# Optimization experiments

Measured on AMD Instinct MI355X. Metric: run time of the kernel, lower is better.

Reference implementation:

```python
import jax, jax.numpy as jnp
import numpy as np
from jax import lax
from jax.scipy.special import logsumexp

B, T, H, L = 64, 512, 768, 9


def setup_inputs() -> dict:
    key = jax.random.key(0)
    k1, k2, k3, k4, k5 = jax.random.split(key, 5)
    hidden = jax.random.normal(k1, (B, T, H), dtype=jnp.float32)
    W = jax.random.normal(k2, (L, H), dtype=jnp.float32) * 0.02
    b = jnp.zeros((L,), dtype=jnp.float32)
    transitions = jax.random.normal(k3, (L, L), dtype=jnp.float32) * 0.1
    lengths = jax.random.randint(k4, (B,), T // 2, T + 1)
    seq_mask = jnp.arange(T)[None, :] < lengths[:, None]          # [B,T] bool
    labels = jax.random.randint(k5, (B, T), 0, L).astype(jnp.int32)
    labels = jnp.where(seq_mask, labels, -100).astype(jnp.int32)   # -100 = ignore
    attention_mask = seq_mask.astype(jnp.int32)
    return {"hidden": hidden, "W": W, "b": b, "transitions": transitions,
            "labels": labels, "attention_mask": attention_mask}


def _crf_nll(logits, tags, transitions, mask):
    # numerator: joint score of the gold path (no start/end transitions)
    maskf = mask.astype(logits.dtype)
    emit = jnp.take_along_axis(logits, tags[..., None], axis=2)[..., 0]   # [B,T]
    emit_score = (emit * maskf).sum(-1)
    trans = transitions[tags[:, :-1], tags[:, 1:]]                        # [B,T-1]
    trans_score = (trans * maskf[:, 1:]).sum(-1)
    numerator = emit_score + trans_score
    # denominator: forward algorithm (log-sum-exp recurrence over time)
    def step(alpha, xs):
        logit_t, mask_t = xs                                   # [B,L], [B]
        inner = alpha[:, :, None] + transitions[None, :, :] + logit_t[:, None, :]
        new = logsumexp(inner, axis=1)
        return jnp.where(mask_t[:, None], new, alpha), None
    alpha0 = logits[:, 0]                                      # mask[:,0] assumed True
    alpha, _ = lax.scan(step, alpha0,
                        (jnp.transpose(logits[:, 1:], (1, 0, 2)), mask[:, 1:].T))
    denominator = logsumexp(alpha, axis=-1)
    return -(numerator - denominator).sum()


def _viterbi(logits, transitions, mask):
    num_tags = transitions.shape[0]
    identity_bp = jnp.broadcast_to(jnp.arange(num_tags)[None, :], logits.shape[:1] + (num_tags,))

    def vstep(vscore, xs):
        logit_t, mask_t = xs
        inner = vscore[:, :, None] + transitions[None, :, :]   # [B,L_prev,L_cur]
        bp = jnp.argmax(inner, axis=1)                         # [B,L]
        new = jnp.max(inner, axis=1) + logit_t
        vscore = jnp.where(mask_t[:, None], new, vscore)
        bp = jnp.where(mask_t[:, None], bp, identity_bp)       # carry tag through pad
        return vscore, bp

    vscore0 = logits[:, 0]
    vscore, bps = lax.scan(vstep, vscore0,
                           (jnp.transpose(logits[:, 1:], (1, 0, 2)), mask[:, 1:].T))
    last_tag = jnp.argmax(vscore, axis=-1)                     # [B]

    def btstep(tag, bp_t):
        prev = jnp.take_along_axis(bp_t, tag[:, None], axis=1)[:, 0]
        return prev, tag

    first_tag, tags_rest = lax.scan(btstep, last_tag, bps, reverse=True)  # ys[t]=tag_{t+1}
    return jnp.concatenate([first_tag[:, None], tags_rest.T], axis=1)     # [B,T]


def reference(hidden, W, b, transitions, labels, attention_mask):
    mask = (attention_mask != 0) & (labels != -100)            # create_combined_mask
    logits = jnp.einsum('bth,lh->btl', hidden, W) + b          # classifier (dropout=eval)
    tags = jnp.where(labels == -100, 0, labels)                # adjust_labels_for_crf
    loss = _crf_nll(logits, tags, transitions, mask)           # -log_likelihood (summed)
    vtags = _viterbi(logits, transitions, mask)                # [B,T]
    # pad_predictions: prepend -100, shift right, -100 outside the masked span
    bsz = hidden.shape[0]
    neg = jnp.full((bsz, 1), -100, dtype=jnp.int32)
    shifted = jnp.concatenate([neg, vtags[:, :-1].astype(jnp.int32)], axis=1)
    valid = jnp.concatenate([jnp.zeros((bsz, 1), bool), mask[:, :-1]], axis=1)
    predictions = jnp.where(valid, shifted, -100)
    return loss, predictions
```

## Files before the change

### kernel.cpp

```cpp
#include <hip/hip_runtime.h>

#define BATCH 64
#define TLEN  512
#define HDIM  768
#define LTAGS 9

#define WS_LOGD 0
#define WS_LOGF 2359296
#define WS_VM   3538944
#define WS_AM   6193152
#define WS_NUM  6856704
#define WS_LOSS 6857216

__global__ __launch_bounds__(256) void logits_kernel(
    const float* __restrict__ hidden, const float* __restrict__ W,
    const float* __restrict__ bvec, double* __restrict__ logitsD,
    float* __restrict__ logitsF)
{
    __shared__ float sW[LTAGS * HDIM];
    __shared__ float sb[LTAGS];
    const int tid = threadIdx.x;
    for (int i = tid; i < LTAGS * HDIM; i += 256) sW[i] = W[i];
    if (tid < LTAGS) sb[tid] = bvec[tid];
    __syncthreads();

    const int lane = tid & 63;
    const int wave = tid >> 6;
    const int sub  = lane & 7;
    const int rg   = lane >> 3;

    const int rowBase = blockIdx.x * 64 + wave * 16;
    const int r0 = rowBase + rg;
    const int r1 = rowBase + rg + 8;
    const float* h0p = hidden + (size_t)r0 * HDIM;
    const float* h1p = hidden + (size_t)r1 * HDIM;

    double acc0[LTAGS], acc1[LTAGS];
    #pragma unroll
    for (int l = 0; l < LTAGS; ++l) { acc0[l] = 0.0; acc1[l] = 0.0; }

    #pragma unroll 2
    for (int i = 0; i < 24; ++i) {
        const int off = i * 32 + sub * 4;
        const float4 h0 = *(const float4*)(h0p + off);
        const float4 h1 = *(const float4*)(h1p + off);
        #pragma unroll
        for (int l = 0; l < LTAGS; ++l) {
            const float4 w = *(const float4*)&sW[l * HDIM + off];
            float d0 = h0.x * w.x;
            d0 = fmaf(h0.y, w.y, d0); d0 = fmaf(h0.z, w.z, d0); d0 = fmaf(h0.w, w.w, d0);
            float d1 = h1.x * w.x;
            d1 = fmaf(h1.y, w.y, d1); d1 = fmaf(h1.z, w.z, d1); d1 = fmaf(h1.w, w.w, d1);
            acc0[l] += (double)d0;
            acc1[l] += (double)d1;
        }
    }
    #pragma unroll
    for (int l = 0; l < LTAGS; ++l) {
        double v0 = acc0[l], v1 = acc1[l];
        #pragma unroll
        for (int off = 4; off > 0; off >>= 1) {
            v0 += __shfl_down(v0, off);
            v1 += __shfl_down(v1, off);
        }
        acc0[l] = v0; acc1[l] = v1;
    }
    if (sub == 0) {
        #pragma unroll
        for (int l = 0; l < LTAGS; ++l) {
            double v0 = acc0[l] + (double)sb[l];
            double v1 = acc1[l] + (double)sb[l];
            logitsD[(size_t)r0 * LTAGS + l] = v0;
            logitsD[(size_t)r1 * LTAGS + l] = v1;
            logitsF[(size_t)r0 * LTAGS + l] = (float)v0;
            logitsF[(size_t)r1 * LTAGS + l] = (float)v1;
        }
    }
}

__global__ __launch_bounds__(256) void chunk_kernel(
    const float* __restrict__ trans, const int* __restrict__ labels,
    const int* __restrict__ att, const double* __restrict__ logitsD,
    const float* __restrict__ logitsF,
    double* __restrict__ wsVM, float* __restrict__ wsAM,
    double* __restrict__ wsNum)
{
    __shared__ double sT64[81];
    __shared__ float  sE32[81];
    const int tid = threadIdx.x;
    if (tid < 81) { float tv = trans[tid]; sT64[tid] = (double)tv; sE32[tid] = __expf(tv); }
    __syncthreads();

    const int blk = blockIdx.x;
    if (blk < 144) {
        const int gid = blk * 256 + tid;
        const int b   = gid / 576;
        const int rem = gid - b * 576;
        const int c   = rem / 9;
        const int i   = rem - c * 9;

        double M[LTAGS];
        #pragma unroll
        for (int j = 0; j < LTAGS; ++j) M[j] = (i == j) ? 0.0 : -1e300;

        const double* lrow = logitsD + ((size_t)b * TLEN + (c * 8 + 1)) * LTAGS;
        const int* lab = labels + b * TLEN;
        const int* am  = att + b * TLEN;
        const int t0 = c * 8 + 1;

        double lg[LTAGS], lgN[LTAGS];
        #pragma unroll
        for (int j = 0; j < LTAGS; ++j) lg[j] = lrow[j];
        bool mk = (am[t0] != 0) && (lab[t0] != -100);

        for (int s = 0; s < 8; ++s) {
            bool mkN = false;
            const int tn = t0 + s + 1;
            if (s < 7 && tn <= TLEN - 1) {
                const double* ln = lrow + (s + 1) * LTAGS;
                #pragma unroll
                for (int j = 0; j < LTAGS; ++j) lgN[j] = ln[j];
                mkN = (am[tn] != 0) && (lab[tn] != -100);
            }
            double nw[LTAGS];
            #pragma unroll
            for (int j = 0; j < LTAGS; ++j) {
                double bst = M[0] + sT64[j];
                #pragma unroll
                for (int k = 1; k < LTAGS; ++k) {
                    double cnd = M[k] + sT64[k * LTAGS + j];
                    bst = fmax(bst, cnd);
                }
                nw[j] = bst + lg[j];
            }
            #pragma unroll
            for (int j = 0; j < LTAGS; ++j) { M[j] = mk ? nw[j] : M[j]; lg[j] = lgN[j]; }
            mk = mkN;
        }
        double* dst = wsVM + (((size_t)b * 64 + c) * LTAGS + i) * LTAGS;
        #pragma unroll
        for (int j = 0; j < LTAGS; ++j) dst[j] = M[j];
    } else if (blk < 216) {
        const int gid = (blk - 144) * 256 + tid;
        const int b   = gid / 288;
        const int rem = gid - b * 288;
        const int c   = rem / 9;
        const int i   = rem - c * 9;

        float M[LTAGS];
        #pragma unroll
        for (int j = 0; j < LTAGS; ++j) M[j] = (i == j) ? 0.f : -1e30f;

        const float* lrow = logitsF + ((size_t)b * TLEN + (c * 16 + 1)) * LTAGS;
        const int* lab = labels + b * TLEN;
        const int* am  = att + b * TLEN;
        const int t0 = c * 16 + 1;

        float lg[LTAGS], lgN[LTAGS];
        #pragma unroll
        for (int j = 0; j < LTAGS; ++j) lg[j] = lrow[j];
        bool mk = (am[t0] != 0) && (lab[t0] != -100);

        for (int s = 0; s < 16; ++s) {
            bool mkN = false;
            const int tn = t0 + s + 1;
            if (s < 15 && tn <= TLEN - 1) {
                const float* ln = lrow + (s + 1) * LTAGS;
                #pragma unroll
                for (int j = 0; j < LTAGS; ++j) lgN[j] = ln[j];
                mkN = (am[tn] != 0) && (lab[tn] != -100);
            }
            float m = M[0];
            #pragma unroll
            for (int k = 1; k < LTAGS; ++k) m = fmaxf(m, M[k]);
            float P[LTAGS];
            #pragma unroll
            for (int k = 0; k < LTAGS; ++k) P[k] = __expf(M[k] - m);
            float nw[LTAGS];
            #pragma unroll
            for (int j = 0; j < LTAGS; ++j) {
                float sacc = P[0] * sE32[j];
                #pragma unroll
                for (int k = 1; k < LTAGS; ++k) sacc = fmaf(P[k], sE32[k * LTAGS + j], sacc);
                nw[j] = m + __logf(sacc) + lg[j];
            }
            #pragma unroll
            for (int j = 0; j < LTAGS; ++j) { M[j] = mk ? nw[j] : M[j]; lg[j] = lgN[j]; }
            mk = mkN;
        }
        float* dst = wsAM + (((size_t)b * 32 + c) * LTAGS + i) * LTAGS;
        #pragma unroll
        for (int j = 0; j < LTAGS; ++j) dst[j] = M[j];
    } else {
        const int bb   = (blk - 216) * 4 + (tid >> 6);
        const int lane = tid & 63;
        const int* lab = labels + bb * TLEN;
        const int* am  = att + bb * TLEN;
        const double* lrowb = logitsD + (size_t)bb * TLEN * LTAGS;
        double part = 0.0;
        #pragma unroll
        for (int k = 0; k < 8; ++k) {
            const int t = lane + k * 64;
            int lv = lab[t], av = am[t];
            bool mkc = (av != 0) && (lv != -100);
            int tg = (lv == -100) ? 0 : lv;
            if (mkc) part += lrowb[(size_t)t * LTAGS + tg];
            if (t < TLEN - 1) {
                int lv2 = lab[t + 1], av2 = am[t + 1];
                bool mk2 = (av2 != 0) && (lv2 != -100);
                int tg2 = (lv2 == -100) ? 0 : lv2;
                if (mk2) part += sT64[tg * LTAGS + tg2];
            }
        }
        #pragma unroll
        for (int off = 32; off > 0; off >>= 1) part += __shfl_down(part, off);
        if (lane == 0) wsNum[bb] = part;
    }
}

__global__ __launch_bounds__(128) void crf2_kernel(
    const float* __restrict__ trans, const int* __restrict__ labels,
    const int* __restrict__ att, const double* __restrict__ logitsD,
    const double* __restrict__ wsVM, const float* __restrict__ wsAM,
    const double* __restrict__ wsNum, double* __restrict__ wsLoss,
    float* __restrict__ out)
{
    __shared__ __align__(16) double sVM[64 * 81];
    __shared__ __align__(16) float  sAM[32 * 81];
    __shared__ double sVstart[65 * LTAGS];
    __shared__ unsigned long long sBPp[513];
    __shared__ int sTagB[65];
    __shared__ double sT64[81];
    __shared__ unsigned char sMk[513];
    __shared__ double sDen;
    __shared__ int sLast;

    const int b = blockIdx.x, tid = threadIdx.x;
    const int wave = tid >> 6, lane = tid & 63;
    const unsigned long long IDMAP = 0x876543210ull;

    const double2* gVM = (const double2*)(wsVM + (size_t)b * 64 * 81);
    double2* sVM2 = (double2*)sVM;
    for (int i = tid; i < 2592; i += 128) sVM2[i] = gVM[i];
    const float4* gAM = (const float4*)(wsAM + (size_t)b * 32 * 81);
    float4* sAM4 = (float4*)sAM;
    for (int i = tid; i < 648; i += 128) sAM4[i] = gAM[i];

    const int* lab = labels + b * TLEN;
    const int* am  = att + b * TLEN;
    for (int t = tid; t < TLEN; t += 128) {
        int lv = lab[t], av = am[t];
        sMk[t] = (av != 0 && lv != -100) ? 1 : 0;
    }
    if (tid == 0) sMk[TLEN] = 0;
    if (tid < 81) sT64[tid] = (double)trans[tid];
    __syncthreads();

    if (wave == 0) {
        const int j = (lane < LTAGS) ? lane : (LTAGS - 1);
        double v = logitsD[(size_t)b * TLEN * LTAGS + j];
        double Mc[LTAGS], Mn[LTAGS];
        #pragma unroll
        for (int i = 0; i < LTAGS; ++i) Mc[i] = sVM[i * LTAGS + j];
        for (int c = 0; c < 64; ++c) {
            if (c < 63) {
                #pragma unroll
                for (int i = 0; i < LTAGS; ++i) Mn[i] = sVM[(c + 1) * 81 + i * LTAGS + j];
            }
            if (lane < LTAGS) sVstart[c * LTAGS + j] = v;
            double g[LTAGS];
            #pragma unroll
            for (int i = 0; i < LTAGS; ++i) g[i] = __shfl(v, i);
            double bst = g[0] + Mc[0];
            #pragma unroll
            for (int i = 1; i < LTAGS; ++i) bst = fmax(bst, g[i] + Mc[i]);
            v = bst;
            if (c < 63) {
                #pragma unroll
                for (int i = 0; i < LTAGS; ++i) Mc[i] = Mn[i];
            }
        }
        if (lane < LTAGS) sVstart[64 * LTAGS + j] = v;
        double g[LTAGS];
        #pragma unroll
        for (int i = 0; i < LTAGS; ++i) g[i] = __shfl(v, i);
        if (lane == 0) {
            int bi = 0; double bv = g[0];
            #pragma unroll
            for (int i = 1; i < LTAGS; ++i) if (g[i] > bv) { bv = g[i]; bi = i; }
            sLast = bi;
        }
    } else {
        const int j = (lane < LTAGS) ? lane : (LTAGS - 1);
        float v = (float)logitsD[(size_t)b * TLEN * LTAGS + j];
        float Mc[LTAGS], Mn[LTAGS];
        #pragma unroll
        for (int i = 0; i < LTAGS; ++i) Mc[i] = sAM[i * LTAGS + j];
        for (int c = 0; c < 32; ++c) {
            if (c < 31) {
                #pragma unroll
                for (int i = 0; i < LTAGS; ++i) Mn[i] = sAM[(c + 1) * 81 + i * LTAGS + j];
            }
            float g[LTAGS];
            #pragma unroll
            for (int i = 0; i < LTAGS; ++i) g[i] = __shfl(v, i);
            float a[LTAGS];
            #pragma unroll
            for (int i = 0; i < LTAGS; ++i) a[i] = g[i] + Mc[i];
            float m = a[0];
            #pragma unroll
            for (int i = 1; i < LTAGS; ++i) m = fmaxf(m, a[i]);
            float sacc = 0.f;
            #pragma unroll
            for (int i = 0; i < LTAGS; ++i) sacc += __expf(a[i] - m);
            v = m + __logf(sacc);
            if (c < 31) {
                #pragma unroll
                for (int i = 0; i < LTAGS; ++i) Mc[i] = Mn[i];
            }
        }
        float g[LTAGS];
        #pragma unroll
        for (int i = 0; i < LTAGS; ++i) g[i] = __shfl(v, i);
        if (lane == 0) {
            float m = g[0];
            #pragma unroll
            for (int i = 1; i < LTAGS; ++i) m = fmaxf(m, g[i]);
            float sacc = 0.f;
            #pragma unroll
            for (int i = 0; i < LTAGS; ++i) sacc += __expf(g[i] - m);
            sDen = (double)(m + __logf(sacc));
        }
    }
    __syncthreads();

    unsigned long long S = IDMAP;
    if (tid < 64) {
        const int c = tid;
        double v[LTAGS];
        #pragma unroll
        for (int j = 0; j < LTAGS; ++j) v[j] = sVstart[c * LTAGS + j];
        const double* lrow = logitsD + ((size_t)b * TLEN + (c * 8 + 1)) * LTAGS;
        double lg[LTAGS], lgN[LTAGS];
        #pragma unroll
        for (int j = 0; j < LTAGS; ++j) lg[j] = lrow[j];

        for (int s = 0; s < 8; ++s) {
            const int t = c * 8 + 1 + s;
            if (s < 7 && t + 1 <= TLEN - 1) {
                const double* ln = lrow + (s + 1) * LTAGS;
                #pragma unroll
                for (int j = 0; j < LTAGS; ++j) lgN[j] = ln[j];
            }
            const bool mk = (sMk[t] != 0);
            unsigned long long pk = 0;
            double nv[LTAGS];
            #pragma unroll
            for (int j = 0; j < LTAGS; ++j) {
                double bst = v[0] + sT64[j];
                int bi = 0;
                #pragma unroll
                for (int k = 1; k < LTAGS; ++k) {
                    double cnd = v[k] + sT64[k * LTAGS + j];
                    bool gt = cnd > bst;
                    bst = gt ? cnd : bst;
                    bi  = gt ? k : bi;
                }
                nv[j] = bst + lg[j];
                pk |= ((unsigned long long)bi) << (4 * j);
            }
            pk = mk ? pk : IDMAP;
            sBPp[t] = pk;
            #pragma unroll
            for (int j = 0; j < LTAGS; ++j) { v[j] = mk ? nv[j] : v[j]; lg[j] = lgN[j]; }
        }
        unsigned long long G = IDMAP;
        for (int s = 7; s >= 0; --s) {
            const unsigned long long bp = sBPp[c * 8 + 1 + s];
            unsigned long long ng = 0;
            #pragma unroll
            for (int j = 0; j < LTAGS; ++j) {
                int gj = (int)((G >> (4 * j)) & 15);
                int f  = (int)((bp >> (4 * gj)) & 15);
                ng |= ((unsigned long long)f) << (4 * j);
            }
            G = ng;
        }
        S = G;
    }

    #pragma unroll
    for (int d = 1; d < 64; d <<= 1) {
        unsigned long long Sn = __shfl_down(S, d);
        if (wave == 0 && lane + d < 64) {
            unsigned long long R = 0;
            #pragma unroll
            for (int x = 0; x < LTAGS; ++x) {
                int y = (int)((Sn >> (4 * x)) & 15);
                int z = (int)((S >> (4 * y)) & 15);
                R |= ((unsigned long long)z) << (4 * x);
            }
            S = R;
        }
    }
    if (tid < 64) {
        const int lt = sLast;
        sTagB[tid] = (int)((S >> (4 * lt)) & 15);
        if (tid == 0) sTagB[64] = lt;
    }
    __syncthreads();

    if (tid < 64) {
        const int c = tid;
        int cur = sTagB[c + 1];
        float* po = out + 1 + b * TLEN;
        for (int s = 8; s >= 1; --s) {
            const int t = c * 8 + s;
            if (t < TLEN) {
                int nxt = (int)((sBPp[t] >> (4 * cur)) & 15);
                po[t] = sMk[t - 1] ? (float)nxt : -100.f;
                cur = nxt;
            }
        }
    }
    if (tid == 0) {
        out[1 + b * TLEN] = -100.f;
        wsLoss[b] = sDen - wsNum[b];
    }
}

__global__ __launch_bounds__(64) void loss_kernel(
    const double* __restrict__ wsLoss, float* __restrict__ out)
{
    double v = wsLoss[threadIdx.x];
    #pragma unroll
    for (int off = 32; off > 0; off >>= 1) v += __shfl_down(v, off);
    if (threadIdx.x == 0) out[0] = (float)v;
}

extern "C" void kernel_launch(void* const* d_in, const int* in_sizes, int n_in,
                              void* d_out, int out_size, void* d_ws, size_t ws_size,
                              hipStream_t stream)
{
    const float* hidden = (const float*)d_in[0];
    const float* W      = (const float*)d_in[1];
    const float* bvec   = (const float*)d_in[2];
    const float* trans  = (const float*)d_in[3];
    const int*   labels = (const int*)d_in[4];
    const int*   att    = (const int*)d_in[5];
    float* out = (float*)d_out;

    char* ws = (char*)d_ws;
    double* logitsD = (double*)(ws + WS_LOGD);
    float*  logitsF = (float*)(ws + WS_LOGF);
    double* wsVM    = (double*)(ws + WS_VM);
    float*  wsAM    = (float*)(ws + WS_AM);
    double* wsNum   = (double*)(ws + WS_NUM);
    double* wsLoss  = (double*)(ws + WS_LOSS);

    logits_kernel<<<512, 256, 0, stream>>>(hidden, W, bvec, logitsD, logitsF);
    chunk_kernel<<<232, 256, 0, stream>>>(trans, labels, att, logitsD, logitsF,
                                          wsVM, wsAM, wsNum);
    crf2_kernel<<<BATCH, 128, 0, stream>>>(trans, labels, att, logitsD,
                                           wsVM, wsAM, wsNum, wsLoss, out);
    loss_kernel<<<1, 64, 0, stream>>>(wsLoss, out);
}
```

Measured before the change: 217.9 us.

## Fuse chunk and CRF combine kernels into one per-batch block kernel

```diff
diff --git a/kernel.cpp b/kernel.cpp
--- a/kernel.cpp
+++ b/kernel.cpp
@@ -6,16 +6,11 @@
 #define LTAGS 9
 
 #define WS_LOGD 0
-#define WS_LOGF 2359296
-#define WS_VM   3538944
-#define WS_AM   6193152
-#define WS_NUM  6856704
-#define WS_LOSS 6857216
+#define WS_LOSS 2359296
 
 __global__ __launch_bounds__(256) void logits_kernel(
     const float* __restrict__ hidden, const float* __restrict__ W,
-    const float* __restrict__ bvec, double* __restrict__ logitsD,
-    float* __restrict__ logitsF)
+    const float* __restrict__ bvec, double* __restrict__ logitsD)
 {
     __shared__ float sW[LTAGS * HDIM];
     __shared__ float sb[LTAGS];
@@ -68,50 +63,81 @@
     if (sub == 0) {
         #pragma unroll
         for (int l = 0; l < LTAGS; ++l) {
-            double v0 = acc0[l] + (double)sb[l];
-            double v1 = acc1[l] + (double)sb[l];
-            logitsD[(size_t)r0 * LTAGS + l] = v0;
-            logitsD[(size_t)r1 * LTAGS + l] = v1;
-            logitsF[(size_t)r0 * LTAGS + l] = (float)v0;
-            logitsF[(size_t)r1 * LTAGS + l] = (float)v1;
+            logitsD[(size_t)r0 * LTAGS + l] = acc0[l] + (double)sb[l];
+            logitsD[(size_t)r1 * LTAGS + l] = acc1[l] + (double)sb[l];
         }
     }
 }
 
-__global__ __launch_bounds__(256) void chunk_kernel(
+__global__ __launch_bounds__(576) void crf_fused(
     const float* __restrict__ trans, const int* __restrict__ labels,
     const int* __restrict__ att, const double* __restrict__ logitsD,
-    const float* __restrict__ logitsF,
-    double* __restrict__ wsVM, float* __restrict__ wsAM,
-    double* __restrict__ wsNum)
+    double* __restrict__ wsLoss, float* __restrict__ out)
 {
+    __shared__ __align__(16) double sVM[64 * 81];
+    __shared__ __align__(16) float  sAM[32 * 81];
+    __shared__ double sVstart[65 * LTAGS];
+    __shared__ unsigned long long sBPp[513];
     __shared__ double sT64[81];
     __shared__ float  sE32[81];
-    const int tid = threadIdx.x;
+    __shared__ unsigned char sMk[513];
+    __shared__ int sTagB[65];
+    __shared__ double sRedN[9];
+    __shared__ double sNum, sDen;
+    __shared__ int sLast;
+
+    const int b = blockIdx.x, tid = threadIdx.x;
+    const int wave = tid >> 6, lane = tid & 63;
+    const unsigned long long IDMAP = 0x876543210ull;
+
+    const int* lab = labels + b * TLEN;
+    const int* am  = att + b * TLEN;
+    const double* gLD = logitsD + (size_t)b * TLEN * LTAGS;
+
     if (tid < 81) { float tv = trans[tid]; sT64[tid] = (double)tv; sE32[tid] = __expf(tv); }
+    if (tid < TLEN) {
+        int lv = lab[tid], av = am[tid];
+        sMk[tid] = (av != 0 && lv != -100) ? 1 : 0;
+    }
+    if (tid == 0) sMk[TLEN] = 0;
+
+    double part = 0.0;
+    if (tid < TLEN) {
+        const int t = tid;
+        int lv = lab[t], av = am[t];
+        bool mkc = (av != 0) && (lv != -100);
+        int tg = (lv == -100) ? 0 : lv;
+        if (mkc) part += gLD[(size_t)t * LTAGS + tg];
+        if (t < TLEN - 1) {
+            int lv2 = lab[t + 1], av2 = am[t + 1];
+            bool mk2 = (av2 != 0) && (lv2 != -100);
+            int tg2 = (lv2 == -100) ? 0 : lv2;
+            if (mk2) part += (double)trans[tg * LTAGS + tg2];
+        }
+    }
+    #pragma unroll
+    for (int off = 32; off > 0; off >>= 1) part += __shfl_down(part, off);
+    if (lane == 0) sRedN[wave] = part;
     __syncthreads();
-
-    const int blk = blockIdx.x;
-    if (blk < 144) {
-        const int gid = blk * 256 + tid;
-        const int b   = gid / 576;
-        const int rem = gid - b * 576;
-        const int c   = rem / 9;
-        const int i   = rem - c * 9;
-
+    if (tid == 0) {
+        double s = 0.0;
+        for (int w = 0; w < 9; ++w) s += sRedN[w];
+        sNum = s;
+    }
+
+    {
+        const int c = tid / 9, i = tid - 9 * c;
         double M[LTAGS];
         #pragma unroll
         for (int j = 0; j < LTAGS; ++j) M[j] = (i == j) ? 0.0 : -1e300;
 
-        const double* lrow = logitsD + ((size_t)b * TLEN + (c * 8 + 1)) * LTAGS;
-        const int* lab = labels + b * TLEN;
-        const int* am  = att + b * TLEN;
+        const double* lrow = gLD + (size_t)(c * 8 + 1) * LTAGS;
         const int t0 = c * 8 + 1;
 
         double lg[LTAGS], lgN[LTAGS];
         #pragma unroll
         for (int j = 0; j < LTAGS; ++j) lg[j] = lrow[j];
-        bool mk = (am[t0] != 0) && (lab[t0] != -100);
+        bool mk = (sMk[t0] != 0);
 
         for (int s = 0; s < 8; ++s) {
             bool mkN = false;
@@ -120,7 +146,7 @@
                 const double* ln = lrow + (s + 1) * LTAGS;
                 #pragma unroll
                 for (int j = 0; j < LTAGS; ++j) lgN[j] = ln[j];
-                mkN = (am[tn] != 0) && (lab[tn] != -100);
+                mkN = (sMk[tn] != 0);
             }
             double nw[LTAGS];
             #pragma unroll
@@ -137,38 +163,68 @@
             for (int j = 0; j < LTAGS; ++j) { M[j] = mk ? nw[j] : M[j]; lg[j] = lgN[j]; }
             mk = mkN;
         }
-        double* dst = wsVM + (((size_t)b * 64 + c) * LTAGS + i) * LTAGS;
-        #pragma unroll
-        for (int j = 0; j < LTAGS; ++j) dst[j] = M[j];
-    } else if (blk < 216) {
-        const int gid = (blk - 144) * 256 + tid;
-        const int b   = gid / 288;
-        const int rem = gid - b * 288;
-        const int c   = rem / 9;
-        const int i   = rem - c * 9;
-
+        #pragma unroll
+        for (int j = 0; j < LTAGS; ++j) sVM[c * 81 + i * LTAGS + j] = M[j];
+    }
+    __syncthreads();
+
+    if (wave == 0) {
+        const int j = (lane < LTAGS) ? lane : (LTAGS - 1);
+        double v = gLD[j];
+        double Mc[LTAGS], Mn[LTAGS];
+        #pragma unroll
+        for (int i = 0; i < LTAGS; ++i) Mc[i] = sVM[i * LTAGS + j];
+        for (int c = 0; c < 64; ++c) {
+            if (c < 63) {
+                #pragma unroll
+                for (int i = 0; i < LTAGS; ++i) Mn[i] = sVM[(c + 1) * 81 + i * LTAGS + j];
+            }
+            if (lane < LTAGS) sVstart[c * LTAGS + j] = v;
+            double g[LTAGS];
+            #pragma unroll
+            for (int i = 0; i < LTAGS; ++i) g[i] = __shfl(v, i);
+            double bst = g[0] + Mc[0];
+            #pragma unroll
+            for (int i = 1; i < LTAGS; ++i) bst = fmax(bst, g[i] + Mc[i]);
+            v = bst;
+            if (c < 63) {
+                #pragma unroll
+                for (int i = 0; i < LTAGS; ++i) Mc[i] = Mn[i];
+            }
+        }
+        if (lane < LTAGS) sVstart[64 * LTAGS + j] = v;
+        double g[LTAGS];
+        #pragma unroll
+        for (int i = 0; i < LTAGS; ++i) g[i] = __shfl(v, i);
+        if (lane == 0) {
+            int bi = 0; double bv = g[0];
+            #pragma unroll
+            for (int i = 1; i < LTAGS; ++i) if (g[i] > bv) { bv = g[i]; bi = i; }
+            sLast = bi;
+        }
+    } else if (tid >= 64 && tid < 352) {
+        const int idx = tid - 64;
+        const int c = idx / 9, i = idx - 9 * c;
         float M[LTAGS];
         #pragma unroll
         for (int j = 0; j < LTAGS; ++j) M[j] = (i == j) ? 0.f : -1e30f;
 
-        const float* lrow = logitsF + ((size_t)b * TLEN + (c * 16 + 1)) * LTAGS;
-        const int* lab = labels + b * TLEN;
-        const int* am  = att + b * TLEN;
+        const double* lrow = gLD + (size_t)(c * 16 + 1) * LTAGS;
         const int t0 = c * 16 + 1;
 
         float lg[LTAGS], lgN[LTAGS];
         #pragma unroll
-        for (int j = 0; j < LTAGS; ++j) lg[j] = lrow[j];
-        bool mk = (am[t0] != 0) && (lab[t0] != -100);
+        for (int j = 0; j < LTAGS; ++j) lg[j] = (float)lrow[j];
+        bool mk = (sMk[t0] != 0);
 
         for (int s = 0; s < 16; ++s) {
             bool mkN = false;
             const int tn = t0 + s + 1;
             if (s < 15 && tn <= TLEN - 1) {
-                const float* ln = lrow + (s + 1) * LTAGS;
-                #pragma unroll
-                for (int j = 0; j < LTAGS; ++j) lgN[j] = ln[j];
-                mkN = (am[tn] != 0) && (lab[tn] != -100);
+                const double* ln = lrow + (s + 1) * LTAGS;
+                #pragma unroll
+                for (int j = 0; j < LTAGS; ++j) lgN[j] = (float)ln[j];
+                mkN = (sMk[tn] != 0);
             }
             float m = M[0];
             #pragma unroll
@@ -188,159 +244,18 @@
             for (int j = 0; j < LTAGS; ++j) { M[j] = mk ? nw[j] : M[j]; lg[j] = lgN[j]; }
             mk = mkN;
         }
-        float* dst = wsAM + (((size_t)b * 32 + c) * LTAGS + i) * LTAGS;
-        #pragma unroll
-        for (int j = 0; j < LTAGS; ++j) dst[j] = M[j];
-    } else {
-        const int bb   = (blk - 216) * 4 + (tid >> 6);
-        const int lane = tid & 63;
-        const int* lab = labels + bb * TLEN;
-        const int* am  = att + bb * TLEN;
-        const double* lrowb = logitsD + (size_t)bb * TLEN * LTAGS;
-        double part = 0.0;
-        #pragma unroll
-        for (int k = 0; k < 8; ++k) {
-            const int t = lane + k * 64;
-            int lv = lab[t], av = am[t];
-            bool mkc = (av != 0) && (lv != -100);
-            int tg = (lv == -100) ? 0 : lv;
-            if (mkc) part += lrowb[(size_t)t * LTAGS + tg];
-            if (t < TLEN - 1) {
-                int lv2 = lab[t + 1], av2 = am[t + 1];
-                bool mk2 = (av2 != 0) && (lv2 != -100);
-                int tg2 = (lv2 == -100) ? 0 : lv2;
-                if (mk2) part += sT64[tg * LTAGS + tg2];
-            }
-        }
-        #pragma unroll
-        for (int off = 32; off > 0; off >>= 1) part += __shfl_down(part, off);
-        if (lane == 0) wsNum[bb] = part;
-    }
-}
-
-__global__ __launch_bounds__(128) void crf2_kernel(
-    const float* __restrict__ trans, const int* __restrict__ labels,
-    const int* __restrict__ att, const double* __restrict__ logitsD,
-    const double* __restrict__ wsVM, const float* __restrict__ wsAM,
-    const double* __restrict__ wsNum, double* __restrict__ wsLoss,
-    float* __restrict__ out)
-{
-    __shared__ __align__(16) double sVM[64 * 81];
-    __shared__ __align__(16) float  sAM[32 * 81];
-    __shared__ double sVstart[65 * LTAGS];
-    __shared__ unsigned long long sBPp[513];
-    __shared__ int sTagB[65];
-    __shared__ double sT64[81];
-    __shared__ unsigned char sMk[513];
-    __shared__ double sDen;
-    __shared__ int sLast;
-
-    const int b = blockIdx.x, tid = threadIdx.x;
-    const int wave = tid >> 6, lane = tid & 63;
-    const unsigned long long IDMAP = 0x876543210ull;
-
-    const double2* gVM = (const double2*)(wsVM + (size_t)b * 64 * 81);
-    double2* sVM2 = (double2*)sVM;
-    for (int i = tid; i < 2592; i += 128) sVM2[i] = gVM[i];
-    const float4* gAM = (const float4*)(wsAM + (size_t)b * 32 * 81);
-    float4* sAM4 = (float4*)sAM;
-    for (int i = tid; i < 648; i += 128) sAM4[i] = gAM[i];
-
-    const int* lab = labels + b * TLEN;
-    const int* am  = att + b * TLEN;
-    for (int t = tid; t < TLEN; t += 128) {
-        int lv = lab[t], av = am[t];
-        sMk[t] = (av != 0 && lv != -100) ? 1 : 0;
-    }
-    if (tid == 0) sMk[TLEN] = 0;
-    if (tid < 81) sT64[tid] = (double)trans[tid];
+        #pragma unroll
+        for (int j = 0; j < LTAGS; ++j) sAM[c * 81 + i * LTAGS + j] = M[j];
+    }
     __syncthreads();
 
+    unsigned long long S = IDMAP;
     if (wave == 0) {
-        const int j = (lane < LTAGS) ? lane : (LTAGS - 1);
-        double v = logitsD[(size_t)b * TLEN * LTAGS + j];
-        double Mc[LTAGS], Mn[LTAGS];
-        #pragma unroll
-        for (int i = 0; i < LTAGS; ++i) Mc[i] = sVM[i * LTAGS + j];
-        for (int c = 0; c < 64; ++c) {
-            if (c < 63) {
-                #pragma unroll
-                for (int i = 0; i < LTAGS; ++i) Mn[i] = sVM[(c + 1) * 81 + i * LTAGS + j];
-            }
-            if (lane < LTAGS) sVstart[c * LTAGS + j] = v;
-            double g[LTAGS];
-            #pragma unroll
-            for (int i = 0; i < LTAGS; ++i) g[i] = __shfl(v, i);
-            double bst = g[0] + Mc[0];
-            #pragma unroll
-            for (int i = 1; i < LTAGS; ++i) bst = fmax(bst, g[i] + Mc[i]);
-            v = bst;
-            if (c < 63) {
-                #pragma unroll
-                for (int i = 0; i < LTAGS; ++i) Mc[i] = Mn[i];
-            }
-        }
-        if (lane < LTAGS) sVstart[64 * LTAGS + j] = v;
-        double g[LTAGS];
-        #pragma unroll
-        for (int i = 0; i < LTAGS; ++i) g[i] = __shfl(v, i);
-        if (lane == 0) {
-            int bi = 0; double bv = g[0];
-            #pragma unroll
-            for (int i = 1; i < LTAGS; ++i) if (g[i] > bv) { bv = g[i]; bi = i; }
-            sLast = bi;
-        }
-    } else {
-        const int j = (lane < LTAGS) ? lane : (LTAGS - 1);
-        float v = (float)logitsD[(size_t)b * TLEN * LTAGS + j];
-        float Mc[LTAGS], Mn[LTAGS];
-        #pragma unroll
-        for (int i = 0; i < LTAGS; ++i) Mc[i] = sAM[i * LTAGS + j];
-        for (int c = 0; c < 32; ++c) {
-            if (c < 31) {
-                #pragma unroll
-                for (int i = 0; i < LTAGS; ++i) Mn[i] = sAM[(c + 1) * 81 + i * LTAGS + j];
-            }
-            float g[LTAGS];
-            #pragma unroll
-            for (int i = 0; i < LTAGS; ++i) g[i] = __shfl(v, i);
-            float a[LTAGS];
-            #pragma unroll
-            for (int i = 0; i < LTAGS; ++i) a[i] = g[i] + Mc[i];
-            float m = a[0];
-            #pragma unroll
-            for (int i = 1; i < LTAGS; ++i) m = fmaxf(m, a[i]);
-            float sacc = 0.f;
-            #pragma unroll
-            for (int i = 0; i < LTAGS; ++i) sacc += __expf(a[i] - m);
-            v = m + __logf(sacc);
-            if (c < 31) {
-                #pragma unroll
-                for (int i = 0; i < LTAGS; ++i) Mc[i] = Mn[i];
-            }
-        }
-        float g[LTAGS];
-        #pragma unroll
-        for (int i = 0; i < LTAGS; ++i) g[i] = __shfl(v, i);
-        if (lane == 0) {
-            float m = g[0];
-            #pragma unroll
-            for (int i = 1; i < LTAGS; ++i) m = fmaxf(m, g[i]);
-            float sacc = 0.f;
-            #pragma unroll
-            for (int i = 0; i < LTAGS; ++i) sacc += __expf(g[i] - m);
-            sDen = (double)(m + __logf(sacc));
-        }
-    }
-    __syncthreads();
-
-    unsigned long long S = IDMAP;
-    if (tid < 64) {
         const int c = tid;
         double v[LTAGS];
         #pragma unroll
         for (int j = 0; j < LTAGS; ++j) v[j] = sVstart[c * LTAGS + j];
-        const double* lrow = logitsD + ((size_t)b * TLEN + (c * 8 + 1)) * LTAGS;
+        const double* lrow = gLD + (size_t)(c * 8 + 1) * LTAGS;
         double lg[LTAGS], lgN[LTAGS];
         #pragma unroll
         for (int j = 0; j < LTAGS; ++j) lg[j] = lrow[j];
@@ -387,6 +302,47 @@
             G = ng;
         }
         S = G;
+    } else if (wave == 1) {
+        const int j = (lane < LTAGS) ? lane : (LTAGS - 1);
+        float v = (float)gLD[j];
+        float Mc[LTAGS], Mn[LTAGS];
+        #pragma unroll
+        for (int i = 0; i < LTAGS; ++i) Mc[i] = sAM[i * LTAGS + j];
+        for (int c = 0; c < 32; ++c) {
+            if (c < 31) {
+                #pragma unroll
+                for (int i = 0; i < LTAGS; ++i) Mn[i] = sAM[(c + 1) * 81 + i * LTAGS + j];
+            }
+            float g[LTAGS];
+            #pragma unroll
+            for (int i = 0; i < LTAGS; ++i) g[i] = __shfl(v, i);
+            float a[LTAGS];
+            #pragma unroll
+            for (int i = 0; i < LTAGS; ++i) a[i] = g[i] + Mc[i];
+            float m = a[0];
+            #pragma unroll
+            for (int i = 1; i < LTAGS; ++i) m = fmaxf(m, a[i]);
+            float sacc = 0.f;
+            #pragma unroll
+            for (int i = 0; i < LTAGS; ++i) sacc += __expf(a[i] - m);
+            v = m + __logf(sacc);
+            if (c < 31) {
+                #pragma unroll
+                for (int i = 0; i < LTAGS; ++i) Mc[i] = Mn[i];
+            }
+        }
+        float g[LTAGS];
+        #pragma unroll
+        for (int i = 0; i < LTAGS; ++i) g[i] = __shfl(v, i);
+        if (lane == 0) {
+            float m = g[0];
+            #pragma unroll
+            for (int i = 1; i < LTAGS; ++i) m = fmaxf(m, g[i]);
+            float sacc = 0.f;
+            #pragma unroll
+            for (int i = 0; i < LTAGS; ++i) sacc += __expf(g[i] - m);
+            sDen = (double)(m + __logf(sacc));
+        }
     }
 
     #pragma unroll
@@ -403,14 +359,12 @@
             S = R;
         }
     }
-    if (tid < 64) {
+
+    if (wave == 0) {
         const int lt = sLast;
         sTagB[tid] = (int)((S >> (4 * lt)) & 15);
         if (tid == 0) sTagB[64] = lt;
-    }
-    __syncthreads();
-
-    if (tid < 64) {
+
         const int c = tid;
         int cur = sTagB[c + 1];
         float* po = out + 1 + b * TLEN;
@@ -423,9 +377,10 @@
             }
         }
     }
+    __syncthreads();
     if (tid == 0) {
         out[1 + b * TLEN] = -100.f;
-        wsLoss[b] = sDen - wsNum[b];
+        wsLoss[b] = sDen - sNum;
     }
 }
 
@@ -452,16 +407,9 @@
 
     char* ws = (char*)d_ws;
     double* logitsD = (double*)(ws + WS_LOGD);
-    float*  logitsF = (float*)(ws + WS_LOGF);
-    double* wsVM    = (double*)(ws + WS_VM);
-    float*  wsAM    = (float*)(ws + WS_AM);
-    double* wsNum   = (double*)(ws + WS_NUM);
     double* wsLoss  = (double*)(ws + WS_LOSS);
 
-    logits_kernel<<<512, 256, 0, stream>>>(hidden, W, bvec, logitsD, logitsF);
-    chunk_kernel<<<232, 256, 0, stream>>>(trans, labels, att, logitsD, logitsF,
-                                          wsVM, wsAM, wsNum);
-    crf2_kernel<<<BATCH, 128, 0, stream>>>(trans, labels, att, logitsD,
-                                           wsVM, wsAM, wsNum, wsLoss, out);
+    logits_kernel<<<512, 256, 0, stream>>>(hidden, W, bvec, logitsD);
+    crf_fused<<<BATCH, 576, 0, stream>>>(trans, labels, att, logitsD, wsLoss, out);
     loss_kernel<<<1, 64, 0, stream>>>(wsLoss, out);
 }
```

After: 280.3 us. 1.29x slower.
